# Performance work log

Hardware: AMD Instinct MI355X
Metric: run time of the kernel (lower is better)

The kernel has to match this reference:

```python
import jax, jax.numpy as jnp
import numpy as np

NUM_EXPERTS = 16
EFF_THRESHOLD = 0.1
SIM_THRESHOLD = 0.0
EPS = 1e-8


def setup_inputs() -> dict:
    key = jax.random.key(0)
    k1, k2 = jax.random.split(key)
    B, E, H = 4096, NUM_EXPERTS, 1024
    rp = jax.random.uniform(k1, (B, E), dtype=jnp.float32)
    rp = rp / rp.sum(axis=-1, keepdims=True)  # valid probabilities
    emb = jax.random.normal(k2, (B, H), dtype=jnp.float32)
    return {"routing_probs": rp, "input_embeddings": emb}


def _total_loss(routing_probs, input_embeddings):
    B, E = routing_probs.shape

    # --- LoadBalanceLoss: var(mean usage) / (1/E)^2, unbiased var (torch default)
    usage = routing_probs.mean(axis=0)                      # [E]
    var = jnp.sum((usage - usage.mean()) ** 2) / (E - 1)
    load_balance = var * (E ** 2)

    # --- EntropyRegularizationLoss (target None): -mean entropy
    entropy = -jnp.sum(routing_probs * jnp.log(routing_probs + EPS), axis=-1)
    entropy_loss = -entropy.mean()

    # --- EfficiencyLoss: sum of probs below threshold, averaged over batch
    small = jnp.where(routing_probs < EFF_THRESHOLD, routing_probs, 0.0)
    efficiency = small.sum(axis=-1).mean()

    # --- ConsistencyLoss: mean KL(softmax(p_j) || softmax(p_i)) over similar pairs
    logp = jax.nn.log_softmax(routing_probs, axis=-1)       # [B, E]
    q = jnp.exp(logp)                                       # [B, E]
    neg_ent_q = jnp.sum(q * logp, axis=-1)                  # [B], = sum q log q
    # KL[i, j] = sum_e q_j (log q_j - logp_i) = neg_ent_q[j] - logp_i . q_j
    kl = neg_ent_q[None, :] - jnp.einsum('ie,je->ij', logp, q)  # [B, B]

    nemb = input_embeddings / jnp.linalg.norm(input_embeddings, axis=-1, keepdims=True)
    sim = nemb @ nemb.T                                     # [B, B]
    mask = (sim > SIM_THRESHOLD) & (~jnp.eye(B, dtype=bool))
    num_pairs = mask.sum()
    cons_sum = jnp.sum(jnp.where(mask, kl, 0.0))
    consistency = jnp.where(num_pairs > 0,
                            cons_sum / jnp.maximum(num_pairs, 1).astype(kl.dtype),
                            0.0)

    return load_balance + entropy_loss + efficiency + consistency


def reference(routing_probs, input_embeddings):
    return _total_loss(routing_probs, input_embeddings)
```

## Files before the change

### kernel.cpp

```cpp
#include <hip/hip_runtime.h>
#include <hip/hip_bf16.h>

#define BROWS 4096
#define NE    16
#define HDIM  1024
#define ACC_F 512
#define NTILE 32
#define NBLK  (NTILE * (NTILE + 1) / 2)
#define PLANE 262144
#define EMBQ_BYTES 4194304

typedef __attribute__((ext_vector_type(8)))  short short8;
typedef __attribute__((ext_vector_type(4)))  float float4v;
typedef __attribute__((ext_vector_type(16))) float float16v;
typedef __attribute__((ext_vector_type(4)))  int   int4v;
typedef __attribute__((ext_vector_type(8)))  int   int8v;

__device__ __forceinline__ unsigned bf16rne(float f) {
    const unsigned u = __float_as_uint(f);
    return (u + 0x7FFFu + ((u >> 16) & 1u)) >> 16;
}
__device__ __forceinline__ unsigned pk2(float lo, float hi) {
    return bf16rne(lo) | (bf16rne(hi) << 16);
}

__device__ __forceinline__ unsigned e4m3(float x) {
    unsigned u = __float_as_uint(x);
    const unsigned s = (u >> 24) & 0x80u;
    u &= 0x7FFFFFFFu;
    if (u >= 0x43E80000u) return s | 0x7Eu;
    u += 0x7FFFFu + ((u >> 20) & 1u);
    const int e = (int)(u >> 23) - 120;
    if (e <= 0) return s;
    return s | ((unsigned)e << 3) | ((u >> 20) & 7u);
}

__device__ __forceinline__ void gl16(const unsigned char* g, unsigned char* l) {
    __builtin_amdgcn_global_load_lds(
        (const __attribute__((address_space(1))) unsigned int*)(unsigned long long)g,
        (__attribute__((address_space(3))) unsigned int*)(unsigned int)(unsigned long long)l,
        16, 0, 0);
}

__device__ __forceinline__ void row16f(const float* src, float* p) {
    const float4v* pv = (const float4v*)src;
    float4v a0 = pv[0], a1 = pv[1], a2 = pv[2], a3 = pv[3];
    p[0]=a0.x; p[1]=a0.y; p[2]=a0.z; p[3]=a0.w;
    p[4]=a1.x; p[5]=a1.y; p[6]=a1.z; p[7]=a1.w;
    p[8]=a2.x; p[9]=a2.y; p[10]=a2.z; p[11]=a2.w;
    p[12]=a3.x; p[13]=a3.y; p[14]=a3.z; p[15]=a3.w;
}

__device__ __forceinline__ void lsm16(const float* p, float* lp, float* q, float& ne) {
    float m = p[0];
#pragma unroll
    for (int e = 1; e < 16; e++) m = fmaxf(m, p[e]);
    float s = 0.f;
#pragma unroll
    for (int e = 0; e < 16; e++) s += expf(p[e] - m);
    const float ls = logf(s);
    ne = 0.f;
#pragma unroll
    for (int e = 0; e < 16; e++) {
        lp[e] = p[e] - m - ls;
        q[e]  = expf(lp[e]);
        ne   += q[e] * lp[e];
    }
}

__device__ __forceinline__ void st8pair(unsigned char* tile, int row, int cp, uint4 v) {
    const int x = row & 7;
    unsigned long long lo = ((unsigned long long)v.y << 32) | v.x;
    unsigned long long hi = ((unsigned long long)v.w << 32) | v.z;
    *(unsigned long long*)(tile + row * 64 + (((2 * cp)     ^ x) << 3)) = lo;
    *(unsigned long long*)(tile + row * 64 + (((2 * cp + 1) ^ x) << 3)) = hi;
}

__device__ __forceinline__ void decode_pair(int id, int& bi, int& bj) {
    int L = (id & 7) * 66 + (id >> 3);
    int gi = 0, gj = 0;
    for (;;) {
        const int cnt = (gi == gj) ? 10 : 16;
        if (L < cnt) break;
        L -= cnt;
        gj++; if (gj == 8) { gi++; gj = gi; }
    }
    if (gi == gj) {
        int u = 0, c = 4;
        while (L >= c) { L -= c; u++; c--; }
        bi = gi * 4 + u; bj = gj * 4 + u + L;
    } else {
        bi = gi * 4 + (L >> 2); bj = gj * 4 + (L & 3);
    }
}

__global__ __launch_bounds__(256) void conv_init(
    const float* __restrict__ src, unsigned char* __restrict__ dst,
    const float* __restrict__ rp, unsigned char* __restrict__ aug,
    float* __restrict__ acc, int nconv)
{
    __shared__ float sred[72];
    const int t = threadIdx.x;
    const int bid = (int)blockIdx.x;
    if (bid == 0 && t < 96) acc[t] = 0.f;
    if (bid < nconv) {
        const size_t k = ((size_t)bid * 256 + t) * 8;
        float4v a = *(const float4v*)(src + k);
        float4v b = *(const float4v*)(src + k + 4);
        unsigned lo = e4m3(a.x) | (e4m3(a.y) << 8) | (e4m3(a.z) << 16) | (e4m3(a.w) << 24);
        unsigned hi = e4m3(b.x) | (e4m3(b.y) << 8) | (e4m3(b.z) << 16) | (e4m3(b.w) << 24);
        *(unsigned long long*)(dst + k) = ((unsigned long long)hi << 32) | lo;
    } else if (nconv > 0) {
        const int pb  = bid - nconv;
        const int row = pb * 256 + t;
        const int lane = t & 63, wid = t >> 6;
        float p[16], lp[16], q[16], ne;
        row16f(rp + (size_t)row * NE, p);
        lsm16(p, lp, q, ne);
        const uint4 z4 = {0u, 0u, 0u, 0u};
        {
            uint4* d = (uint4*)(aug + (size_t)row * 64);
            uint4 w0 = {pk2(lp[0],lp[1]), pk2(lp[2],lp[3]), pk2(lp[4],lp[5]), pk2(lp[6],lp[7])};
            uint4 w1 = {pk2(lp[8],lp[9]), pk2(lp[10],lp[11]), pk2(lp[12],lp[13]), pk2(lp[14],lp[15])};
            uint4 w2 = {pk2(1.f, 0.f), 0u, 0u, 0u};
            d[0] = w0; d[1] = w1; d[2] = w2; d[3] = z4;
        }
        {
            uint4* d = (uint4*)(aug + PLANE + (size_t)row * 64);
            uint4 w0 = {pk2(q[0],q[1]), pk2(q[2],q[3]), pk2(q[4],q[5]), pk2(q[6],q[7])};
            uint4 w1 = {pk2(q[8],q[9]), pk2(q[10],q[11]), pk2(q[12],q[13]), pk2(q[14],q[15])};
            uint4 w2 = {pk2(ne, 0.f), 0u, 0u, 0u};
            d[0] = w0; d[1] = w1; d[2] = w2; d[3] = z4;
        }
        {
            uint4* d = (uint4*)(aug + 2 * PLANE + (size_t)row * 64);
            uint4 w0 = {pk2(-q[0],-q[1]), pk2(-q[2],-q[3]), pk2(-q[4],-q[5]), pk2(-q[6],-q[7])};
            uint4 w1 = {pk2(-q[8],-q[9]), pk2(-q[10],-q[11]), pk2(-q[12],-q[13]), pk2(-q[14],-q[15])};
            uint4 w2 = {pk2(ne, 0.f), 0u, 0u, 0u};
            d[0] = w0; d[1] = w1; d[2] = w2; d[3] = z4;
        }
        {
            uint4* d = (uint4*)(aug + 3 * PLANE + (size_t)row * 64);
            uint4 w0 = {pk2(-lp[0],-lp[1]), pk2(-lp[2],-lp[3]), pk2(-lp[4],-lp[5]), pk2(-lp[6],-lp[7])};
            uint4 w1 = {pk2(-lp[8],-lp[9]), pk2(-lp[10],-lp[11]), pk2(-lp[12],-lp[13]), pk2(-lp[14],-lp[15])};
            uint4 w2 = {pk2(1.f, 0.f), 0u, 0u, 0u};
            d[0] = w0; d[1] = w1; d[2] = w2; d[3] = z4;
        }
        float ent = 0.f, eff = 0.f;
#pragma unroll
        for (int e = 0; e < 16; e++) {
            ent += p[e] * logf(p[e] + 1e-8f);
            if (p[e] < 0.1f) eff += p[e];
        }
        float vals[18];
#pragma unroll
        for (int e = 0; e < 16; e++) vals[e] = p[e];
        vals[16] = ent; vals[17] = eff;
#pragma unroll
        for (int e = 0; e < 18; e++) {
#pragma unroll
            for (int o = 32; o > 0; o >>= 1) vals[e] += __shfl_down(vals[e], o);
        }
        if (lane == 0) {
#pragma unroll
            for (int e = 0; e < 18; e++) sred[wid * 18 + e] = vals[e];
        }
        __syncthreads();
        if (t < 18)
            acc[96 + pb * 18 + t] = sred[t] + sred[18 + t] + sred[36 + t] + sred[54 + t];
    }
}

template<bool PRE>
__global__ __launch_bounds__(1024, 4) void gram_kl(
    const float* __restrict__ embf, const unsigned char* __restrict__ embq,
    const float* __restrict__ rp, const unsigned char* __restrict__ aug,
    float* __restrict__ acc, unsigned int* __restrict__ out)
{
    __shared__ char smem[65536];
    int bi, bj;
    decode_pair((int)blockIdx.x, bi, bj);
    const int t = threadIdx.x;
    const int lane = t & 63, wid = t >> 6;

    if constexpr (PRE) {
        const int wi0 = (wid >> 2) * 32, wj0 = (wid & 3) * 32;
        const int l31 = lane & 31, lhi = lane >> 5;
        float16v accG;
#pragma unroll
        for (int r = 0; r < 16; ++r) accG[r] = 0.f;

        int roA[2][2], roB[2][2];
        {
            const int rA = wi0 + l31;
            const int rB = wj0 + l31;
#pragma unroll
            for (int c = 0; c < 2; ++c)
#pragma unroll
                for (int e = 0; e < 2; ++e) {
                    const int u = c * 4 + lhi * 2 + e;
                    roA[c][e] = rA * 128 + ((u ^ (rA & 7)) << 4);
                    roB[c][e] = rB * 128 + ((u ^ (rB & 7)) << 4);
                }
        }
        const int rg = wid * 8 + (lane >> 3);
        const int gu = (lane & 7) ^ (lane >> 3);
        const unsigned char* gA = embq + (size_t)(bi * 128 + rg) * 1024 + (gu << 4);
        const unsigned char* gB = embq + (size_t)(bj * 128 + rg) * 1024 + (gu << 4);
        const int ldoff = wid * 1024;

        gl16(gA, (unsigned char*)smem + ldoff);
        gl16(gB, (unsigned char*)smem + 16384 + ldoff);
        for (int T = 0; T < 8; ++T) {
            unsigned char* cur = (unsigned char*)smem + (T & 1) * 32768;
            unsigned char* nxt = (unsigned char*)smem + ((T + 1) & 1) * 32768;
            __syncthreads();
            if (T < 7) {
                const int kt = (T + 1) * 128;
                gl16(gA + kt, nxt + ldoff);
                gl16(gB + kt, nxt + 16384 + ldoff);
            }
            unsigned char* curB = cur + 16384;
#pragma unroll
            for (int c = 0; c < 2; ++c) {
                int4v a0 = *(const int4v*)(cur + roA[c][0]);
                int4v a1 = *(const int4v*)(cur + roA[c][1]);
                int4v b0 = *(const int4v*)(curB + roB[c][0]);
                int4v b1 = *(const int4v*)(curB + roB[c][1]);
                int8v A = {a0[0], a0[1], a0[2], a0[3], a1[0], a1[1], a1[2], a1[3]};
                int8v B = {b0[0], b0[1], b0[2], b0[3], b1[0], b1[1], b1[2], b1[3]};
                accG = __builtin_amdgcn_mfma_scale_f32_32x32x64_f8f6f4(
                    A, B, accG, 0, 0, 0, 0x7F7F7F7F, 0, 0x7F7F7F7F);
            }
        }
        __syncthreads();

        const unsigned char* AFp = aug;
        const unsigned char* ARp = aug + PLANE;
        const unsigned char* BFp = aug + 2 * PLANE;
        const unsigned char* BRp = aug + 3 * PLANE;
        float klacc = 0.f, cntacc = 0.f;
        const bool offd = (bi != bj);
        {
            const size_t ra = (size_t)(bi * 128 + wi0 + l31) * 64 + (size_t)(lhi << 4);
            short8 af0 = *(const short8*)(AFp + ra);
            short8 af1 = *(const short8*)(AFp + ra + 32);
            short8 ar0 = *(const short8*)(ARp + ra);
            short8 ar1 = *(const short8*)(ARp + ra + 32);
            const int jg0 = bj * 128 + wj0 + l31;
            const size_t rb = (size_t)jg0 * 64 + (size_t)(lhi << 4);
            short8 bfr0 = *(const short8*)(BFp + rb);
            short8 bfr1 = *(const short8*)(BFp + rb + 32);
            short8 brr0 = *(const short8*)(BRp + rb);
            short8 brr1 = *(const short8*)(BRp + rb + 32);
            float16v zz;
#pragma unroll
            for (int r = 0; r < 16; ++r) zz[r] = 0.f;
            float16v aF = __builtin_amdgcn_mfma_f32_32x32x16_bf16(af0, bfr0, zz, 0, 0, 0);
            aF = __builtin_amdgcn_mfma_f32_32x32x16_bf16(af1, bfr1, aF, 0, 0, 0);
            float16v aR = __builtin_amdgcn_mfma_f32_32x32x16_bf16(ar0, brr0, zz, 0, 0, 0);
            aR = __builtin_amdgcn_mfma_f32_32x32x16_bf16(ar1, brr1, aR, 0, 0, 0);
#pragma unroll
            for (int r = 0; r < 16; ++r) {
                const int ig = bi * 128 + wi0 + (r & 3) + 8 * (r >> 2) + 4 * lhi;
                const float g = accG[r];
                if ((g > 0.f) && (ig != jg0)) {
                    klacc  += aF[r];
                    cntacc += 1.f;
                    if (offd) { klacc += aR[r]; cntacc += 1.f; }
                }
            }
        }

#pragma unroll
        for (int o = 32; o > 0; o >>= 1) {
            klacc  += __shfl_down(klacc, o);
            cntacc += __shfl_down(cntacc, o);
        }
        float* red = (float*)smem;
        float* F1  = (float*)(smem + 256);
        float* F2  = (float*)(smem + 512);
        int*  pisl = (int*)(smem + 2048);
        if (lane == 0) { red[wid] = klacc; red[16 + wid] = cntacc; }
        __syncthreads();
        if (t == 0) {
            float k = 0.f, c = 0.f;
#pragma unroll
            for (int w = 0; w < 16; w++) { k += red[w]; c += red[16 + w]; }
            atomicAdd(&acc[18 + ((int)blockIdx.x & 31)], k);
            atomicAdd(&acc[50 + ((int)blockIdx.x & 31)], c);
            const unsigned got = __hip_atomic_fetch_add((unsigned int*)(acc + 82), 1u,
                                                        __ATOMIC_RELEASE, __HIP_MEMORY_SCOPE_AGENT);
            pisl[0] = (got == NBLK - 1) ? 1 : 0;
        }
        __syncthreads();

        if (pisl[0]) {
            if (t == 0)
                (void)__hip_atomic_load((unsigned int*)(acc + 82), __ATOMIC_ACQUIRE,
                                        __HIP_MEMORY_SCOPE_AGENT);
            __syncthreads();
            if (t < 64)
                F1[t] = __hip_atomic_load(&acc[18 + t], __ATOMIC_RELAXED, __HIP_MEMORY_SCOPE_AGENT);
            if (t < 288)
                F2[t] = __hip_atomic_load(&acc[96 + t], __ATOMIC_RELAXED, __HIP_MEMORY_SCOPE_AGENT);
            __syncthreads();
            if (t == 0) {
                float u[16], usum = 0.f, ents = 0.f, effs = 0.f;
#pragma unroll
                for (int e = 0; e < 16; e++) u[e] = 0.f;
                for (int b = 0; b < 16; b++) {
#pragma unroll
                    for (int e = 0; e < 16; e++) u[e] += F2[b * 18 + e];
                    ents += F2[b * 18 + 16];
                    effs += F2[b * 18 + 17];
                }
#pragma unroll
                for (int e = 0; e < 16; e++) { u[e] /= (float)BROWS; usum += u[e]; }
                const float mean = usum / 16.f;
                float var = 0.f;
#pragma unroll
                for (int e = 0; e < 16; e++) { float dd = u[e] - mean; var += dd * dd; }
                var /= 15.f;
                const float lb  = var * 256.f;
                const float ent = ents / (float)BROWS;
                const float eff = effs / (float)BROWS;
                float kl = 0.f, cnt = 0.f;
#pragma unroll
                for (int s = 0; s < 32; s++) { kl += F1[s]; cnt += F1[32 + s]; }
                const float cons = (cnt > 0.f) ? (kl / fmaxf(cnt, 1.f)) : 0.f;
                const float total = lb + ent + eff + cons;
                const unsigned fb   = __float_as_uint(total);
                const unsigned hi   = fb >> 16;
                const unsigned mant = fb & 0xFFFFu;
                const unsigned rnd  = (mant > 0x8000u || (mant == 0x8000u && (hi & 1))) ? 1u : 0u;
                out[0] = (fb & 0xFFFF0000u) | ((hi + rnd) & 0xFFFFu);
            }
        }
    } else {
        const int wi0 = (wid >> 1) * 32, wj0 = (wid & 1) * 64;
        __hip_bfloat16* eAF = (__hip_bfloat16*)smem;
        __hip_bfloat16* eBF = (__hip_bfloat16*)(smem + 8192);
        __hip_bfloat16* eAR = (__hip_bfloat16*)(smem + 16384);
        __hip_bfloat16* eBR = (__hip_bfloat16*)(smem + 24576);
        float* red  = (float*)(smem + 40960);
        int*   pisl = (int*)(smem + 41024);
        float* fin  = (float*)(smem + 41088);
        const int lrow = lane & 15, quad = lane >> 4;

        float4v accf[2][4];
#pragma unroll
        for (int a = 0; a < 2; a++)
#pragma unroll
            for (int b = 0; b < 4; b++) { accf[a][b].x=0.f; accf[a][b].y=0.f; accf[a][b].z=0.f; accf[a][b].w=0.f; }

        int roA[2][2], roB[4][2];
#pragma unroll
        for (int f = 0; f < 2; f++) {
            const int r = wi0 + f * 16 + lrow;
#pragma unroll
            for (int s = 0; s < 2; s++) roA[f][s] = r * 64 + (((s * 4 + quad) ^ (r & 7)) << 3);
        }
#pragma unroll
        for (int f = 0; f < 4; f++) {
            const int r = wj0 + f * 16 + lrow;
#pragma unroll
            for (int s = 0; s < 2; s++) roB[f][s] = r * 64 + (((s * 4 + quad) ^ (r & 7)) << 3);
        }
        const int row = t >> 2, cp = t & 3;
        const float* gA = embf + (size_t)(bi * 128 + row) * HDIM + cp * 16;
        const float* gB = embf + (size_t)(bj * 128 + row) * HDIM + cp * 16;
        for (int T = 0; T < 16; ++T) {
            const int kt = T * 64;
            unsigned char* bufA = (unsigned char*)(smem + (T & 1) * 16384);
            unsigned char* bufB = bufA + 8192;
            uint4 wa, wb;
            {
                float4v x0 = *(const float4v*)(gA + kt),      x1 = *(const float4v*)(gA + kt + 4);
                float4v x2 = *(const float4v*)(gA + kt + 8),  x3 = *(const float4v*)(gA + kt + 12);
                wa.x = e4m3(x0.x) | (e4m3(x0.y)<<8) | (e4m3(x0.z)<<16) | (e4m3(x0.w)<<24);
                wa.y = e4m3(x1.x) | (e4m3(x1.y)<<8) | (e4m3(x1.z)<<16) | (e4m3(x1.w)<<24);
                wa.z = e4m3(x2.x) | (e4m3(x2.y)<<8) | (e4m3(x2.z)<<16) | (e4m3(x2.w)<<24);
                wa.w = e4m3(x3.x) | (e4m3(x3.y)<<8) | (e4m3(x3.z)<<16) | (e4m3(x3.w)<<24);
                float4v y0 = *(const float4v*)(gB + kt),      y1 = *(const float4v*)(gB + kt + 4);
                float4v y2 = *(const float4v*)(gB + kt + 8),  y3 = *(const float4v*)(gB + kt + 12);
                wb.x = e4m3(y0.x) | (e4m3(y0.y)<<8) | (e4m3(y0.z)<<16) | (e4m3(y0.w)<<24);
                wb.y = e4m3(y1.x) | (e4m3(y1.y)<<8) | (e4m3(y1.z)<<16) | (e4m3(y1.w)<<24);
                wb.z = e4m3(y2.x) | (e4m3(y2.y)<<8) | (e4m3(y2.z)<<16) | (e4m3(y2.w)<<24);
                wb.w = e4m3(y3.x) | (e4m3(y3.y)<<8) | (e4m3(y3.z)<<16) | (e4m3(y3.w)<<24);
            }
            st8pair(bufA, row, cp, wa);
            st8pair(bufB, row, cp, wb);
            __syncthreads();
#pragma unroll
            for (int s = 0; s < 2; s++) {
                long a0 = *(const long*)(bufA + roA[0][s]);
                long a1 = *(const long*)(bufA + roA[1][s]);
                long b0 = *(const long*)(bufB + roB[0][s]);
                long b1 = *(const long*)(bufB + roB[1][s]);
                long b2 = *(const long*)(bufB + roB[2][s]);
                long b3 = *(const long*)(bufB + roB[3][s]);
                accf[0][0] = __builtin_amdgcn_mfma_f32_16x16x32_fp8_fp8(a0, b0, accf[0][0], 0, 0, 0);
                accf[0][1] = __builtin_amdgcn_mfma_f32_16x16x32_fp8_fp8(a0, b1, accf[0][1], 0, 0, 0);
                accf[0][2] = __builtin_amdgcn_mfma_f32_16x16x32_fp8_fp8(a0, b2, accf[0][2], 0, 0, 0);
                accf[0][3] = __builtin_amdgcn_mfma_f32_16x16x32_fp8_fp8(a0, b3, accf[0][3], 0, 0, 0);
                accf[1][0] = __builtin_amdgcn_mfma_f32_16x16x32_fp8_fp8(a1, b0, accf[1][0], 0, 0, 0);
                accf[1][1] = __builtin_amdgcn_mfma_f32_16x16x32_fp8_fp8(a1, b1, accf[1][1], 0, 0, 0);
                accf[1][2] = __builtin_amdgcn_mfma_f32_16x16x32_fp8_fp8(a1, b2, accf[1][2], 0, 0, 0);
                accf[1][3] = __builtin_amdgcn_mfma_f32_16x16x32_fp8_fp8(a1, b3, accf[1][3], 0, 0, 0);
            }
            __syncthreads();
        }
        __syncthreads();

        {
            float p[16], lp[16], q[16], ne;
            const bool iSide = (t < 128);
            if (t < 256) {
                const int rloc = iSide ? t : (t - 128);
                const int grow = (iSide ? bi : bj) * 128 + rloc;
                row16f(rp + (size_t)grow * NE, p);
                lsm16(p, lp, q, ne);
                float r1[16], r2[16], x1, x2;
                if (iSide) {
#pragma unroll
                    for (int e = 0; e < 16; e++) { r1[e] = lp[e]; r2[e] = q[e]; }
                    x1 = 1.f; x2 = ne;
                } else {
#pragma unroll
                    for (int e = 0; e < 16; e++) { r1[e] = -q[e]; r2[e] = -lp[e]; }
                    x1 = ne; x2 = 1.f;
                }
                const int s = (rloc >> 1) & 3;
                __hip_bfloat16* d1 = (iSide ? eAF : eBF) + rloc * 32;
                __hip_bfloat16* d2 = (iSide ? eAR : eBR) + rloc * 32;
                uint4 w0 = {pk2(r1[0],r1[1]), pk2(r1[2],r1[3]), pk2(r1[4],r1[5]), pk2(r1[6],r1[7])};
                uint4 w1 = {pk2(r1[8],r1[9]), pk2(r1[10],r1[11]), pk2(r1[12],r1[13]), pk2(r1[14],r1[15])};
                uint4 w2 = {pk2(x1, 0.f), 0u, 0u, 0u};
                uint4 w3 = {0u, 0u, 0u, 0u};
                *(uint4*)(d1 + (0 ^ s) * 8) = w0;
                *(uint4*)(d1 + (1 ^ s) * 8) = w1;
                *(uint4*)(d1 + (2 ^ s) * 8) = w2;
                *(uint4*)(d1 + (3 ^ s) * 8) = w3;
                uint4 v0 = {pk2(r2[0],r2[1]), pk2(r2[2],r2[3]), pk2(r2[4],r2[5]), pk2(r2[6],r2[7])};
                uint4 v1 = {pk2(r2[8],r2[9]), pk2(r2[10],r2[11]), pk2(r2[12],r2[13]), pk2(r2[14],r2[15])};
                uint4 v2 = {pk2(x2, 0.f), 0u, 0u, 0u};
                *(uint4*)(d2 + (0 ^ s) * 8) = v0;
                *(uint4*)(d2 + (1 ^ s) * 8) = v1;
                *(uint4*)(d2 + (2 ^ s) * 8) = v2;
                *(uint4*)(d2 + (3 ^ s) * 8) = w3;
            }
            if (bi == bj && iSide) {
                float ent = 0.f, eff = 0.f;
#pragma unroll
                for (int e = 0; e < 16; e++) {
                    ent += p[e] * logf(p[e] + 1e-8f);
                    if (p[e] < 0.1f) eff += p[e];
                }
#pragma unroll
                for (int e = 0; e < 18; e++) {
                    float v = (e < 16) ? p[e] : ((e == 16) ? ent : eff);
#pragma unroll
                    for (int o = 32; o > 0; o >>= 1) v += __shfl_down(v, o);
                    if (lane == 0) atomicAdd(&acc[e], v);
                }
            }
        }
        __syncthreads();

        int eoA[2], eoB[4];
#pragma unroll
        for (int f = 0; f < 2; f++) {
            const int r = wi0 + f * 16 + lrow;
            eoA[f] = r * 32 + (quad ^ ((r >> 1) & 3)) * 8;
        }
#pragma unroll
        for (int f = 0; f < 4; f++) {
            const int r = wj0 + f * 16 + lrow;
            eoB[f] = r * 32 + (quad ^ ((r >> 1) & 3)) * 8;
        }

        float4v accF[2][4], accR[2][4];
        {
            const float4v z = {0.f, 0.f, 0.f, 0.f};
            short8 af[2], ar[2], bfr[4], brr[4];
#pragma unroll
            for (int f = 0; f < 2; f++) {
                af[f] = *(const short8*)(eAF + eoA[f]);
                ar[f] = *(const short8*)(eAR + eoA[f]);
            }
#pragma unroll
            for (int f = 0; f < 4; f++) {
                bfr[f] = *(const short8*)(eBF + eoB[f]);
                brr[f] = *(const short8*)(eBR + eoB[f]);
            }
#pragma unroll
            for (int fi = 0; fi < 2; fi++)
#pragma unroll
                for (int fj = 0; fj < 4; fj++) {
                    accF[fi][fj] = __builtin_amdgcn_mfma_f32_16x16x32_bf16(af[fi], bfr[fj], z, 0, 0, 0);
                    accR[fi][fj] = __builtin_amdgcn_mfma_f32_16x16x32_bf16(ar[fi], brr[fj], z, 0, 0, 0);
                }
        }

        float klacc = 0.f, cntacc = 0.f;
        const bool offd = (bi != bj);
#pragma unroll
        for (int fi = 0; fi < 2; fi++) {
#pragma unroll
            for (int fj = 0; fj < 4; fj++) {
#pragma unroll
                for (int rg = 0; rg < 4; rg++) {
                    const int ig = bi * 128 + wi0 + fi * 16 + quad * 4 + rg;
                    const int jg = bj * 128 + wj0 + fj * 16 + lrow;
                    const float g = accf[fi][fj][rg];
                    if ((g > 0.f) && (ig != jg)) {
                        klacc  += accF[fi][fj][rg];
                        cntacc += 1.f;
                        if (offd) { klacc += accR[fi][fj][rg]; cntacc += 1.f; }
                    }
                }
            }
        }

#pragma unroll
        for (int o = 32; o > 0; o >>= 1) {
            klacc  += __shfl_down(klacc, o);
            cntacc += __shfl_down(cntacc, o);
        }
        if (lane == 0) { red[wid] = klacc; red[8 + wid] = cntacc; }
        __syncthreads();
        if (t == 0) {
            float k = 0.f, c = 0.f;
#pragma unroll
            for (int w = 0; w < 8; w++) { k += red[w]; c += red[8 + w]; }
            atomicAdd(&acc[18 + ((int)blockIdx.x & 31)], k);
            atomicAdd(&acc[50 + ((int)blockIdx.x & 31)], c);
            const unsigned got = __hip_atomic_fetch_add((unsigned int*)(acc + 82), 1u,
                                                        __ATOMIC_RELEASE, __HIP_MEMORY_SCOPE_AGENT);
            pisl[0] = (got == NBLK - 1) ? 1 : 0;
        }
        __syncthreads();

        if (pisl[0]) {
            if (t == 0)
                (void)__hip_atomic_load((unsigned int*)(acc + 82), __ATOMIC_ACQUIRE,
                                        __HIP_MEMORY_SCOPE_AGENT);
            __syncthreads();
            if (t < 82)
                fin[t] = __hip_atomic_load(&acc[t], __ATOMIC_RELAXED, __HIP_MEMORY_SCOPE_AGENT);
            __syncthreads();
            if (t == 0) {
                float u[16], usum = 0.f;
#pragma unroll
                for (int e = 0; e < 16; e++) { u[e] = fin[e] / (float)BROWS; usum += u[e]; }
                const float mean = usum / 16.f;
                float var = 0.f;
#pragma unroll
                for (int e = 0; e < 16; e++) { float dd = u[e] - mean; var += dd * dd; }
                var /= 15.f;
                const float lb  = var * 256.f;
                const float ent = fin[16] / (float)BROWS;
                const float eff = fin[17] / (float)BROWS;
                float kl = 0.f, cnt = 0.f;
#pragma unroll
                for (int s = 0; s < 32; s++) { kl += fin[18 + s]; cnt += fin[50 + s]; }
                const float cons = (cnt > 0.f) ? (kl / fmaxf(cnt, 1.f)) : 0.f;
                const float total = lb + ent + eff + cons;
                const unsigned fb   = __float_as_uint(total);
                const unsigned hi   = fb >> 16;
                const unsigned mant = fb & 0xFFFFu;
                const unsigned rnd  = (mant > 0x8000u || (mant == 0x8000u && (hi & 1))) ? 1u : 0u;
                out[0] = (fb & 0xFFFF0000u) | ((hi + rnd) & 0xFFFFu);
            }
        }
    }
}

extern "C" void kernel_launch(void* const* d_in, const int* in_sizes, int n_in,
                              void* d_out, int out_size, void* d_ws, size_t ws_size,
                              hipStream_t stream) {
    const float* rp  = (const float*)d_in[0];
    const float* emb = (const float*)d_in[1];
    float* acc = (float*)d_ws;
    unsigned char* embq = (unsigned char*)d_ws + ACC_F * sizeof(float);
    unsigned char* aug  = embq + EMBQ_BYTES;
    (void)in_sizes; (void)n_in; (void)out_size;

    const size_t need = ACC_F * sizeof(float) + EMBQ_BYTES + 4 * (size_t)PLANE;
    const bool pre = (ws_size >= need);

    if (pre) {
        const int nconv = (BROWS * HDIM) / (256 * 8);
        conv_init<<<nconv + 16, 256, 0, stream>>>(emb, embq, rp, aug, acc, nconv);
        gram_kl<true><<<NBLK, 1024, 0, stream>>>(emb, embq, rp, aug, acc, (unsigned int*)d_out);
    } else {
        conv_init<<<1, 256, 0, stream>>>(emb, nullptr, nullptr, nullptr, acc, 0);
        gram_kl<false><<<NBLK, 512, 0, stream>>>(emb, nullptr, rp, nullptr, acc,
                                                 (unsigned int*)d_out);
    }
}
```

Measured before the change: 127.8 us.

## Load FP8 gram operands directly from global memory, dropping LDS staging

The PRE gram path no longer stages the FP8 embedding tiles through double-buffered LDS with global_load_lds and per-step barriers. Each lane now reads its 32-byte MFMA operands straight from global memory. LDS use shrinks to a small reduction buffer, which can raise occupancy and removes the barriers from the main loop. The reverse-KL MFMA and its operand loads are also skipped on diagonal blocks. The cost is that each operand row is re-read from global or L2 by several waves instead of once per block, and the per-lane accesses are strided.

```diff
diff --git a/kernel.cpp b/kernel.cpp
--- a/kernel.cpp
+++ b/kernel.cpp
@@ -13,7 +13,6 @@
 typedef __attribute__((ext_vector_type(8)))  short short8;
 typedef __attribute__((ext_vector_type(4)))  float float4v;
 typedef __attribute__((ext_vector_type(16))) float float16v;
-typedef __attribute__((ext_vector_type(4)))  int   int4v;
 typedef __attribute__((ext_vector_type(8)))  int   int8v;
 
 __device__ __forceinline__ unsigned bf16rne(float f) {
@@ -33,13 +32,6 @@
     const int e = (int)(u >> 23) - 120;
     if (e <= 0) return s;
     return s | ((unsigned)e << 3) | ((u >> 20) & 7u);
-}
-
-__device__ __forceinline__ void gl16(const unsigned char* g, unsigned char* l) {
-    __builtin_amdgcn_global_load_lds(
-        (const __attribute__((address_space(1))) unsigned int*)(unsigned long long)g,
-        (__attribute__((address_space(3))) unsigned int*)(unsigned int)(unsigned long long)l,
-        16, 0, 0);
 }
 
 __device__ __forceinline__ void row16f(const float* src, float* p) {
@@ -177,98 +169,73 @@
     const float* __restrict__ rp, const unsigned char* __restrict__ aug,
     float* __restrict__ acc, unsigned int* __restrict__ out)
 {
-    __shared__ char smem[65536];
     int bi, bj;
     decode_pair((int)blockIdx.x, bi, bj);
     const int t = threadIdx.x;
     const int lane = t & 63, wid = t >> 6;
 
     if constexpr (PRE) {
+        __shared__ float sred[384];
+        __shared__ int   islast;
         const int wi0 = (wid >> 2) * 32, wj0 = (wid & 3) * 32;
         const int l31 = lane & 31, lhi = lane >> 5;
+
+        const unsigned char* pA = embq + (size_t)(bi * 128 + wi0 + l31) * 1024 + (lhi << 5);
+        const unsigned char* pB = embq + (size_t)(bj * 128 + wj0 + l31) * 1024 + (lhi << 5);
         float16v accG;
 #pragma unroll
         for (int r = 0; r < 16; ++r) accG[r] = 0.f;
-
-        int roA[2][2], roB[2][2];
-        {
-            const int rA = wi0 + l31;
-            const int rB = wj0 + l31;
-#pragma unroll
-            for (int c = 0; c < 2; ++c)
-#pragma unroll
-                for (int e = 0; e < 2; ++e) {
-                    const int u = c * 4 + lhi * 2 + e;
-                    roA[c][e] = rA * 128 + ((u ^ (rA & 7)) << 4);
-                    roB[c][e] = rB * 128 + ((u ^ (rB & 7)) << 4);
-                }
-        }
-        const int rg = wid * 8 + (lane >> 3);
-        const int gu = (lane & 7) ^ (lane >> 3);
-        const unsigned char* gA = embq + (size_t)(bi * 128 + rg) * 1024 + (gu << 4);
-        const unsigned char* gB = embq + (size_t)(bj * 128 + rg) * 1024 + (gu << 4);
-        const int ldoff = wid * 1024;
-
-        gl16(gA, (unsigned char*)smem + ldoff);
-        gl16(gB, (unsigned char*)smem + 16384 + ldoff);
+#pragma unroll
         for (int T = 0; T < 8; ++T) {
-            unsigned char* cur = (unsigned char*)smem + (T & 1) * 32768;
-            unsigned char* nxt = (unsigned char*)smem + ((T + 1) & 1) * 32768;
-            __syncthreads();
-            if (T < 7) {
-                const int kt = (T + 1) * 128;
-                gl16(gA + kt, nxt + ldoff);
-                gl16(gB + kt, nxt + 16384 + ldoff);
-            }
-            unsigned char* curB = cur + 16384;
 #pragma unroll
             for (int c = 0; c < 2; ++c) {
-                int4v a0 = *(const int4v*)(cur + roA[c][0]);
-                int4v a1 = *(const int4v*)(cur + roA[c][1]);
-                int4v b0 = *(const int4v*)(curB + roB[c][0]);
-                int4v b1 = *(const int4v*)(curB + roB[c][1]);
-                int8v A = {a0[0], a0[1], a0[2], a0[3], a1[0], a1[1], a1[2], a1[3]};
-                int8v B = {b0[0], b0[1], b0[2], b0[3], b1[0], b1[1], b1[2], b1[3]};
+                const int off = T * 128 + c * 64;
+                int8v A = *(const int8v*)(pA + off);
+                int8v B = *(const int8v*)(pB + off);
                 accG = __builtin_amdgcn_mfma_scale_f32_32x32x64_f8f6f4(
                     A, B, accG, 0, 0, 0, 0x7F7F7F7F, 0, 0x7F7F7F7F);
             }
         }
-        __syncthreads();
 
         const unsigned char* AFp = aug;
         const unsigned char* ARp = aug + PLANE;
         const unsigned char* BFp = aug + 2 * PLANE;
         const unsigned char* BRp = aug + 3 * PLANE;
+        const int jg0 = bj * 128 + wj0 + l31;
+        const size_t ra = (size_t)(bi * 128 + wi0 + l31) * 64 + (size_t)(lhi << 4);
+        const size_t rb = (size_t)jg0 * 64 + (size_t)(lhi << 4);
+        const bool offd = (bi != bj);
         float klacc = 0.f, cntacc = 0.f;
-        const bool offd = (bi != bj);
-        {
-            const size_t ra = (size_t)(bi * 128 + wi0 + l31) * 64 + (size_t)(lhi << 4);
+        {
             short8 af0 = *(const short8*)(AFp + ra);
             short8 af1 = *(const short8*)(AFp + ra + 32);
+            short8 bf0 = *(const short8*)(BFp + rb);
+            short8 bf1 = *(const short8*)(BFp + rb + 32);
+            float16v zz;
+#pragma unroll
+            for (int r = 0; r < 16; ++r) zz[r] = 0.f;
+            float16v aF = __builtin_amdgcn_mfma_f32_32x32x16_bf16(af0, bf0, zz, 0, 0, 0);
+            aF = __builtin_amdgcn_mfma_f32_32x32x16_bf16(af1, bf1, aF, 0, 0, 0);
+#pragma unroll
+            for (int r = 0; r < 16; ++r) {
+                const int ig = bi * 128 + wi0 + (r & 3) + 8 * (r >> 2) + 4 * lhi;
+                if ((accG[r] > 0.f) && (ig != jg0)) { klacc += aF[r]; cntacc += 1.f; }
+            }
+        }
+        if (offd) {
             short8 ar0 = *(const short8*)(ARp + ra);
             short8 ar1 = *(const short8*)(ARp + ra + 32);
-            const int jg0 = bj * 128 + wj0 + l31;
-            const size_t rb = (size_t)jg0 * 64 + (size_t)(lhi << 4);
-            short8 bfr0 = *(const short8*)(BFp + rb);
-            short8 bfr1 = *(const short8*)(BFp + rb + 32);
-            short8 brr0 = *(const short8*)(BRp + rb);
-            short8 brr1 = *(const short8*)(BRp + rb + 32);
+            short8 br0 = *(const short8*)(BRp + rb);
+            short8 br1 = *(const short8*)(BRp + rb + 32);
             float16v zz;
 #pragma unroll
             for (int r = 0; r < 16; ++r) zz[r] = 0.f;
-            float16v aF = __builtin_amdgcn_mfma_f32_32x32x16_bf16(af0, bfr0, zz, 0, 0, 0);
-            aF = __builtin_amdgcn_mfma_f32_32x32x16_bf16(af1, bfr1, aF, 0, 0, 0);
-            float16v aR = __builtin_amdgcn_mfma_f32_32x32x16_bf16(ar0, brr0, zz, 0, 0, 0);
-            aR = __builtin_amdgcn_mfma_f32_32x32x16_bf16(ar1, brr1, aR, 0, 0, 0);
+            float16v aR = __builtin_amdgcn_mfma_f32_32x32x16_bf16(ar0, br0, zz, 0, 0, 0);
+            aR = __builtin_amdgcn_mfma_f32_32x32x16_bf16(ar1, br1, aR, 0, 0, 0);
 #pragma unroll
             for (int r = 0; r < 16; ++r) {
                 const int ig = bi * 128 + wi0 + (r & 3) + 8 * (r >> 2) + 4 * lhi;
-                const float g = accG[r];
-                if ((g > 0.f) && (ig != jg0)) {
-                    klacc  += aF[r];
-                    cntacc += 1.f;
-                    if (offd) { klacc += aR[r]; cntacc += 1.f; }
-                }
+                if ((accG[r] > 0.f) && (ig != jg0)) { klacc += aR[r]; cntacc += 1.f; }
             }
         }
 
@@ -277,10 +244,9 @@
             klacc  += __shfl_down(klacc, o);
             cntacc += __shfl_down(cntacc, o);
         }
-        float* red = (float*)smem;
-        float* F1  = (float*)(smem + 256);
-        float* F2  = (float*)(smem + 512);
-        int*  pisl = (int*)(smem + 2048);
+        float* red = sred;
+        float* F1  = sred + 32;
+        float* F2  = sred + 96;
         if (lane == 0) { red[wid] = klacc; red[16 + wid] = cntacc; }
         __syncthreads();
         if (t == 0) {
@@ -291,11 +257,11 @@
             atomicAdd(&acc[50 + ((int)blockIdx.x & 31)], c);
             const unsigned got = __hip_atomic_fetch_add((unsigned int*)(acc + 82), 1u,
                                                         __ATOMIC_RELEASE, __HIP_MEMORY_SCOPE_AGENT);
-            pisl[0] = (got == NBLK - 1) ? 1 : 0;
-        }
-        __syncthreads();
-
-        if (pisl[0]) {
+            islast = (got == NBLK - 1) ? 1 : 0;
+        }
+        __syncthreads();
+
+        if (islast) {
             if (t == 0)
                 (void)__hip_atomic_load((unsigned int*)(acc + 82), __ATOMIC_ACQUIRE,
                                         __HIP_MEMORY_SCOPE_AGENT);
@@ -338,6 +304,7 @@
             }
         }
     } else {
+        __shared__ char smem[65536];
         const int wi0 = (wid >> 1) * 32, wj0 = (wid & 1) * 64;
         __hip_bfloat16* eAF = (__hip_bfloat16*)smem;
         __hip_bfloat16* eBF = (__hip_bfloat16*)(smem + 8192);
```

Result: slower. 192.1 us (+50.3%).
